# Kernel optimization log

Measured on AMD Instinct MI355X. Metric: run time of the kernel, lower is better.

The kernel has to match this reference:

```python
import jax, jax.numpy as jnp
import numpy as np

EPS = 1e-6
N, CHANNEL, M, K, D = 4096, 1024, 8, 2048, 128


def setup_inputs() -> dict:
    key = jax.random.key(0)
    ks = jax.random.split(key, 7)
    std = float(np.sqrt(2.0 / (5.0 * CHANNEL / M)))  # matches nn.init.normal_ std in __init__
    return {
        "x": jax.random.normal(ks[0], (N, CHANNEL), dtype=jnp.float32),
        "codebook0": jax.random.normal(ks[1], (M, K, D), dtype=jnp.float32) * std,
        "codebook1": jax.random.normal(ks[2], (M, K, D), dtype=jnp.float32) * std,
        "temperature0": jnp.ones((M, 1), dtype=jnp.float32),
        "temperature1": jnp.ones((M, 1), dtype=jnp.float32),
        "u0": jax.random.uniform(ks[3], (N, M, K), dtype=jnp.float32),
        "u1": jax.random.uniform(ks[4], (N, M, K), dtype=jnp.float32),
    }


def _distance(z, codebook):
    # z: (n, m, d), codebook: (m, k, d) -> (n, m, k) squared euclidean
    x2 = jnp.sum(z * z, axis=-1, keepdims=True)          # (n, m, 1)
    c2 = jnp.sum(codebook * codebook, axis=-1)           # (m, k)
    inter = jnp.einsum('nmd,mkd->nmk', z, codebook)      # (n, m, k)
    return x2 + c2 - 2.0 * inter


def _level(x, codebook, temperature, u):
    # One _quantizerEncoder level with Identity heads.
    n = x.shape[0]
    m, k, d = codebook.shape
    z = x.reshape(n, m, d)
    scale = jnp.asarray(np.sqrt(k), dtype=x.dtype)
    # logit = -distance / sqrt(k) * LowerBound(temperature, Eps)
    logit = (-_distance(z, codebook) / scale) * jnp.maximum(temperature, EPS)
    # gumbel-softmax, tau=1.0, hard=True (permutationRate == 0 -> no permutation)
    uc = jnp.clip(u, EPS, 1.0 - EPS)
    gumbel = -jnp.log(-jnp.log(uc))
    y = jax.nn.softmax(logit + gumbel, axis=-1)          # (n, m, k)
    hard_idx = jnp.argmax(y, axis=-1)                    # (n, m)
    y_hard = jax.nn.one_hot(hard_idx, k, dtype=y.dtype)
    sample = y_hard + y - jax.lax.stop_gradient(y)       # straight-through
    # _multiCodebookDeQuantization.forward
    deq = jnp.einsum('nmk,mkd->nmd', sample, codebook).reshape(n, m * d)
    return sample, deq, logit


def reference(x, codebook0, codebook1, temperature0, temperature1, u0, u1):
    # Encoder pass (Identity latentStageEncoder/quantizationHead/latentHead)
    _, deq0, _ = _level(x, codebook0, temperature0, u0)
    x1 = x - deq0                                        # residual to next level
    _, deq1, _ = _level(x1, codebook1, temperature1, u1)
    # Decoder pass, reversed (Identity dequantizationHead/sideHead/restoreHead):
    # formerLevel = decode(level1); xHat = deq0 + sideHead(formerLevel)
    former = deq1
    xHat = deq0 + former
    return xHat
```

## Files before the change

kernel.cpp:

```cpp
#include <hip/hip_runtime.h>
#include <math.h>


namespace {
constexpr int Nn = 4096, Mm = 8, Kk = 2048, Dd = 128;
constexpr int MK = Mm * Kk;
constexpr double SQRTK = 45.254833995939045;
constexpr float MARGIN = 0.25f;

__device__ __forceinline__ double wsum_d(double v) {
#pragma unroll
  for (int o = 32; o > 0; o >>= 1) v += __shfl_xor(v, o);
  return v;
}
__device__ __forceinline__ float wsum_f(float v) {
#pragma unroll
  for (int o = 32; o > 0; o >>= 1) v += __shfl_xor(v, o);
  return v;
}
__device__ __forceinline__ float wmax_f(float v) {
#pragma unroll
  for (int o = 32; o > 0; o >>= 1) v = fmaxf(v, __shfl_xor(v, o));
  return v;
}

__device__ __forceinline__ float fast_gumbel(float u) {
  float uc = fminf(fmaxf(u, 1e-6f), 0.999999f);
  float t = -0.69314718f * __log2f(uc);
  return -0.69314718f * __log2f(t);
}
__device__ __forceinline__ double gumbel_d(float u) {
  double uc = fmin(fmax((double)u, 1e-6), 1.0 - 1e-6);
  return -log(-log(uc));
}

__global__ __launch_bounds__(256) void prep_kernel(
    const float* __restrict__ cb0, const float* __restrict__ cb1,
    const float* __restrict__ t0, const float* __restrict__ t1,
    float2* __restrict__ AS0, float2* __restrict__ AS1,
    double* __restrict__ c2d0, double* __restrict__ c2d1) {
  int wid = threadIdx.x >> 6, lane = threadIdx.x & 63;
  int row = blockIdx.x * 4 + wid;
  int lvl = row >= MK;
  int r = row & (MK - 1);
  int m = r >> 11;
  const float* cb = lvl ? cb1 : cb0;
  const float* tp = lvl ? t1 : t0;
  float2 c = ((const float2*)(cb + (size_t)r * Dd))[lane];
  double s = (double)c.x * (double)c.x + (double)c.y * (double)c.y;
  s = wsum_d(s);
  if (lane == 0) {
    float wf = (float)((double)fmaxf(tp[m], 1e-6f) / SQRTK);
    float2 as;
    as.x = (float)s * wf;
    as.y = 2.0f * (float)sqrt(s) * wf;
    if (lvl) { c2d1[r] = s; AS1[r] = as; }
    else     { c2d0[r] = s; AS0[r] = as; }
  }
}

__device__ __forceinline__ int argmax_level(
    float zx, float zy, int lane,
    const float* __restrict__ cbm,
    const float* __restrict__ urow,
    const float2* __restrict__ ASm,
    const double* __restrict__ c2m,
    double wd) {
  float zn = sqrtf(wsum_f(zx * zx + zy * zy));
  const float4* u4 = (const float4*)urow;
  const float4* as4 = (const float4*)ASm;

  float ub[32];
  float lbmax = -1e30f;
#pragma unroll
  for (int j = 0; j < 8; ++j) {
    float4 uu = u4[j * 64 + lane];
    float4 a0 = as4[(j * 64 + lane) * 2];
    float4 a1 = as4[(j * 64 + lane) * 2 + 1];
    float g0 = fast_gumbel(uu.x), g1 = fast_gumbel(uu.y);
    float g2 = fast_gumbel(uu.z), g3 = fast_gumbel(uu.w);
    float s0 = zn * a0.y, s1 = zn * a0.w, s2 = zn * a1.y, s3 = zn * a1.w;
    float b0 = g0 - a0.x, b1 = g1 - a0.z, b2 = g2 - a1.x, b3 = g3 - a1.z;
    ub[j * 4 + 0] = b0 + s0; lbmax = fmaxf(lbmax, b0 - s0);
    ub[j * 4 + 1] = b1 + s1; lbmax = fmaxf(lbmax, b1 - s1);
    ub[j * 4 + 2] = b2 + s2; lbmax = fmaxf(lbmax, b2 - s2);
    ub[j * 4 + 3] = b3 + s3; lbmax = fmaxf(lbmax, b3 - s3);
  }
  float thr = wmax_f(lbmax) - MARGIN;

  unsigned mask32 = 0;
#pragma unroll
  for (int t = 0; t < 32; ++t) mask32 |= (ub[t] >= thr ? 1u : 0u) << t;

  double bestS = -1e300;
  int bestK = 0;
  while (true) {
    unsigned long long wm = __ballot(mask32 != 0);
    if (!wm) break;
    int l = (int)__ffsll(wm) - 1;
    unsigned lm = (unsigned)__shfl((int)mask32, l);
    int t = __builtin_ffs((int)lm) - 1;
    if (lane == l) mask32 &= mask32 - 1;
    int kc = ((t >> 2) << 8) + (l << 2) + (t & 3);
    float2 c = ((const float2*)(cbm + (size_t)kc * Dd))[lane];
    double dot = wsum_d((double)zx * (double)c.x + (double)zy * (double)c.y);
    double sc = (2.0 * dot - c2m[kc]) * wd + gumbel_d(urow[kc]);
    if (sc > bestS) { bestS = sc; bestK = kc; }
  }
  return bestK;
}

__global__ __launch_bounds__(256, 4) void fused_kernel(
    const float* __restrict__ x,
    const float* __restrict__ cb0, const float* __restrict__ cb1,
    const float* __restrict__ t0, const float* __restrict__ t1,
    const float* __restrict__ u0, const float* __restrict__ u1,
    const float2* __restrict__ AS0, const float2* __restrict__ AS1,
    const double* __restrict__ c2d0, const double* __restrict__ c2d1,
    float* __restrict__ out) {
  const int wid = threadIdx.x >> 6, lane = threadIdx.x & 63;
  const int p = blockIdx.x * 4 + wid;
  const int m = p >> 12;
  const int n = p & 4095;

  float2 z = ((const float2*)(x + (size_t)n * 1024 + m * Dd))[lane];
  double wd0 = (double)fmaxf(t0[m], 1e-6f) / SQRTK;
  double wd1 = (double)fmaxf(t1[m], 1e-6f) / SQRTK;

  const float* u0row = u0 + ((size_t)n * Mm + m) * Kk;
  const float* u1row = u1 + ((size_t)n * Mm + m) * Kk;
  const float* cb0m = cb0 + (size_t)m * Kk * Dd;
  const float* cb1m = cb1 + (size_t)m * Kk * Dd;

  int b0 = argmax_level(z.x, z.y, lane, cb0m, u0row, AS0 + m * Kk, c2d0 + m * Kk, wd0);
  float2 c0 = ((const float2*)(cb0m + (size_t)b0 * Dd))[lane];

  float zx1 = z.x - c0.x, zy1 = z.y - c0.y;
  int b1 = argmax_level(zx1, zy1, lane, cb1m, u1row, AS1 + m * Kk, c2d1 + m * Kk, wd1);
  float2 c1 = ((const float2*)(cb1m + (size_t)b1 * Dd))[lane];

  ((float2*)(out + (size_t)n * 1024 + m * Dd))[lane] =
      make_float2(c0.x + c1.x, c0.y + c1.y);
}
}

extern "C" void kernel_launch(void* const* d_in, const int* in_sizes, int n_in,
                              void* d_out, int out_size, void* d_ws, size_t ws_size,
                              hipStream_t stream) {
  const float* x   = (const float*)d_in[0];
  const float* cb0 = (const float*)d_in[1];
  const float* cb1 = (const float*)d_in[2];
  const float* t0  = (const float*)d_in[3];
  const float* t1  = (const float*)d_in[4];
  const float* u0  = (const float*)d_in[5];
  const float* u1  = (const float*)d_in[6];
  float* out = (float*)d_out;

  char* ws = (char*)d_ws;
  float2* AS0 = (float2*)ws;
  float2* AS1 = AS0 + MK;
  double* c2d0 = (double*)(AS1 + MK);
  double* c2d1 = c2d0 + MK;

  prep_kernel<<<8192, 256, 0, stream>>>(cb0, cb1, t0, t1, AS0, AS1, c2d0, c2d1);
  fused_kernel<<<8192, 256, 0, stream>>>(x, cb0, cb1, t0, t1, u0, u1,
                                         AS0, AS1, c2d0, c2d1, out);
}
```

Baseline: 623.3 us.

## Replace per-code bound pruning with global u-threshold from codebook norm ranges

Per-code upper/lower bound arrays are replaced by one per-(level,m) range table, holding the spread of squared norms and the maximum norm, built in a new small reduction kernel. Each row now needs only its maximum uniform sample to derive a threshold on u. Candidates are then selected by comparing raw u values against it, so the per-element gumbel logs and AS table loads go away. The bound is looser, so more candidates may need exact double-precision evaluation, and the launch-bounds occupancy hint is dropped.

After: 569.4 us. -8.6%, faster.

```diff
diff --git a/kernel.cpp b/kernel.cpp
--- a/kernel.cpp
+++ b/kernel.cpp
@@ -3,10 +3,10 @@
 
 
 namespace {
-constexpr int Nn = 4096, Mm = 8, Kk = 2048, Dd = 128;
+constexpr int Mm = 8, Kk = 2048, Dd = 128;
 constexpr int MK = Mm * Kk;
 constexpr double SQRTK = 45.254833995939045;
-constexpr float MARGIN = 0.25f;
+constexpr double MARGIN = 0.05;
 
 __device__ __forceinline__ double wsum_d(double v) {
 #pragma unroll
@@ -24,74 +24,80 @@
   return v;
 }
 
-__device__ __forceinline__ float fast_gumbel(float u) {
-  float uc = fminf(fmaxf(u, 1e-6f), 0.999999f);
-  float t = -0.69314718f * __log2f(uc);
-  return -0.69314718f * __log2f(t);
-}
 __device__ __forceinline__ double gumbel_d(float u) {
   double uc = fmin(fmax((double)u, 1e-6), 1.0 - 1e-6);
   return -log(-log(uc));
 }
 
-__global__ __launch_bounds__(256) void prep_kernel(
+__global__ __launch_bounds__(256) void prep1(
     const float* __restrict__ cb0, const float* __restrict__ cb1,
-    const float* __restrict__ t0, const float* __restrict__ t1,
-    float2* __restrict__ AS0, float2* __restrict__ AS1,
     double* __restrict__ c2d0, double* __restrict__ c2d1) {
   int wid = threadIdx.x >> 6, lane = threadIdx.x & 63;
   int row = blockIdx.x * 4 + wid;
   int lvl = row >= MK;
   int r = row & (MK - 1);
-  int m = r >> 11;
   const float* cb = lvl ? cb1 : cb0;
-  const float* tp = lvl ? t1 : t0;
   float2 c = ((const float2*)(cb + (size_t)r * Dd))[lane];
-  double s = (double)c.x * (double)c.x + (double)c.y * (double)c.y;
-  s = wsum_d(s);
-  if (lane == 0) {
-    float wf = (float)((double)fmaxf(tp[m], 1e-6f) / SQRTK);
-    float2 as;
-    as.x = (float)s * wf;
-    as.y = 2.0f * (float)sqrt(s) * wf;
-    if (lvl) { c2d1[r] = s; AS1[r] = as; }
-    else     { c2d0[r] = s; AS0[r] = as; }
+  double s = wsum_d((double)c.x * (double)c.x + (double)c.y * (double)c.y);
+  if (lane == 0) { if (lvl) c2d1[r] = s; else c2d0[r] = s; }
+}
+
+__global__ __launch_bounds__(256) void prep2(
+    const double* __restrict__ c2d0, const double* __restrict__ c2d1,
+    const float* __restrict__ t0, const float* __restrict__ t1,
+    float2* __restrict__ Rtab) {
+  int b = blockIdx.x;
+  int lvl = b >> 3, m = b & 7;
+  const double* c2 = (lvl ? c2d1 : c2d0) + m * Kk;
+  int tid = threadIdx.x;
+  double mx = -1e300, mn = 1e300;
+  for (int i = tid; i < Kk; i += 256) { double v = c2[i]; mx = fmax(mx, v); mn = fmin(mn, v); }
+#pragma unroll
+  for (int o = 32; o > 0; o >>= 1) {
+    mx = fmax(mx, __shfl_xor(mx, o));
+    mn = fmin(mn, __shfl_xor(mn, o));
+  }
+  __shared__ double smx[4], smn[4];
+  int wid = tid >> 6, lane = tid & 63;
+  if (lane == 0) { smx[wid] = mx; smn[wid] = mn; }
+  __syncthreads();
+  if (tid == 0) {
+    mx = fmax(fmax(smx[0], smx[1]), fmax(smx[2], smx[3]));
+    mn = fmin(fmin(smn[0], smn[1]), fmin(smn[2], smn[3]));
+    double w = (double)fmaxf(lvl ? t1[m] : t0[m], 1e-6f) / SQRTK;
+    float2 r;
+    r.x = (float)(w * (mx - mn) * 1.0001);
+    r.y = (float)(4.0 * w * sqrt(mx) * 1.0001);
+    Rtab[b] = r;
   }
 }
 
-__device__ __forceinline__ int argmax_level(
+__device__ __forceinline__ int do_level(
     float zx, float zy, int lane,
+    const float* __restrict__ urow,
     const float* __restrict__ cbm,
-    const float* __restrict__ urow,
-    const float2* __restrict__ ASm,
     const double* __restrict__ c2m,
-    double wd) {
-  float zn = sqrtf(wsum_f(zx * zx + zy * zy));
+    float2 rr, double wd) {
   const float4* u4 = (const float4*)urow;
-  const float4* as4 = (const float4*)ASm;
-
-  float ub[32];
-  float lbmax = -1e30f;
+  float4 r[8];
+  float um = 0.f;
 #pragma unroll
   for (int j = 0; j < 8; ++j) {
-    float4 uu = u4[j * 64 + lane];
-    float4 a0 = as4[(j * 64 + lane) * 2];
-    float4 a1 = as4[(j * 64 + lane) * 2 + 1];
-    float g0 = fast_gumbel(uu.x), g1 = fast_gumbel(uu.y);
-    float g2 = fast_gumbel(uu.z), g3 = fast_gumbel(uu.w);
-    float s0 = zn * a0.y, s1 = zn * a0.w, s2 = zn * a1.y, s3 = zn * a1.w;
-    float b0 = g0 - a0.x, b1 = g1 - a0.z, b2 = g2 - a1.x, b3 = g3 - a1.z;
-    ub[j * 4 + 0] = b0 + s0; lbmax = fmaxf(lbmax, b0 - s0);
-    ub[j * 4 + 1] = b1 + s1; lbmax = fmaxf(lbmax, b1 - s1);
-    ub[j * 4 + 2] = b2 + s2; lbmax = fmaxf(lbmax, b2 - s2);
-    ub[j * 4 + 3] = b3 + s3; lbmax = fmaxf(lbmax, b3 - s3);
+    r[j] = u4[j * 64 + lane];
+    um = fmaxf(um, fmaxf(fmaxf(r[j].x, r[j].y), fmaxf(r[j].z, r[j].w)));
   }
-  float thr = wmax_f(lbmax) - MARGIN;
-
+  um = wmax_f(um);
+  float zn = sqrtf(wsum_f(zx * zx + zy * zy));
+  double thr = gumbel_d(um) - (double)(rr.x + rr.y * zn) - MARGIN;
+  float uthr = (float)(exp(-exp(-thr)) * (1.0 - 1e-7));
   unsigned mask32 = 0;
 #pragma unroll
-  for (int t = 0; t < 32; ++t) mask32 |= (ub[t] >= thr ? 1u : 0u) << t;
-
+  for (int j = 0; j < 8; ++j) {
+    mask32 |= (r[j].x >= uthr ? 1u : 0u) << (j * 4 + 0);
+    mask32 |= (r[j].y >= uthr ? 1u : 0u) << (j * 4 + 1);
+    mask32 |= (r[j].z >= uthr ? 1u : 0u) << (j * 4 + 2);
+    mask32 |= (r[j].w >= uthr ? 1u : 0u) << (j * 4 + 3);
+  }
   double bestS = -1e300;
   int bestK = 0;
   while (true) {
@@ -105,18 +111,18 @@
     float2 c = ((const float2*)(cbm + (size_t)kc * Dd))[lane];
     double dot = wsum_d((double)zx * (double)c.x + (double)zy * (double)c.y);
     double sc = (2.0 * dot - c2m[kc]) * wd + gumbel_d(urow[kc]);
-    if (sc > bestS) { bestS = sc; bestK = kc; }
+    if (sc > bestS || (sc == bestS && kc < bestK)) { bestS = sc; bestK = kc; }
   }
   return bestK;
 }
 
-__global__ __launch_bounds__(256, 4) void fused_kernel(
+__global__ __launch_bounds__(256) void fused_kernel(
     const float* __restrict__ x,
     const float* __restrict__ cb0, const float* __restrict__ cb1,
     const float* __restrict__ t0, const float* __restrict__ t1,
     const float* __restrict__ u0, const float* __restrict__ u1,
-    const float2* __restrict__ AS0, const float2* __restrict__ AS1,
     const double* __restrict__ c2d0, const double* __restrict__ c2d1,
+    const float2* __restrict__ Rtab,
     float* __restrict__ out) {
   const int wid = threadIdx.x >> 6, lane = threadIdx.x & 63;
   const int p = blockIdx.x * 4 + wid;
@@ -132,11 +138,11 @@
   const float* cb0m = cb0 + (size_t)m * Kk * Dd;
   const float* cb1m = cb1 + (size_t)m * Kk * Dd;
 
-  int b0 = argmax_level(z.x, z.y, lane, cb0m, u0row, AS0 + m * Kk, c2d0 + m * Kk, wd0);
+  int b0 = do_level(z.x, z.y, lane, u0row, cb0m, c2d0 + m * Kk, Rtab[m], wd0);
   float2 c0 = ((const float2*)(cb0m + (size_t)b0 * Dd))[lane];
 
-  float zx1 = z.x - c0.x, zy1 = z.y - c0.y;
-  int b1 = argmax_level(zx1, zy1, lane, cb1m, u1row, AS1 + m * Kk, c2d1 + m * Kk, wd1);
+  int b1 = do_level(z.x - c0.x, z.y - c0.y, lane, u1row, cb1m, c2d1 + m * Kk,
+                    Rtab[8 + m], wd1);
   float2 c1 = ((const float2*)(cb1m + (size_t)b1 * Dd))[lane];
 
   ((float2*)(out + (size_t)n * 1024 + m * Dd))[lane] =
@@ -157,12 +163,12 @@
   float* out = (float*)d_out;
 
   char* ws = (char*)d_ws;
-  float2* AS0 = (float2*)ws;
-  float2* AS1 = AS0 + MK;
-  double* c2d0 = (double*)(AS1 + MK);
+  double* c2d0 = (double*)ws;
   double* c2d1 = c2d0 + MK;
+  float2* Rtab = (float2*)(c2d1 + MK);
 
-  prep_kernel<<<8192, 256, 0, stream>>>(cb0, cb1, t0, t1, AS0, AS1, c2d0, c2d1);
+  prep1<<<8192, 256, 0, stream>>>(cb0, cb1, c2d0, c2d1);
+  prep2<<<16, 256, 0, stream>>>(c2d0, c2d1, t0, t1, Rtab);
   fused_kernel<<<8192, 256, 0, stream>>>(x, cb0, cb1, t0, t1, u0, u1,
-                                         AS0, AS1, c2d0, c2d1, out);
+                                         c2d0, c2d1, Rtab, out);
 }
```
